# Performance work log

Measured on AMD Instinct MI355X. Metric: run time of the kernel, lower is better.

Reference implementation:

```python
import math
import jax, jax.numpy as jnp
import numpy as np

L, D, H, F, V, S = 4, 1024, 16, 4096, 50257, 2048
HS = D // H
EPS = 1e-5
STD = 0.02


def setup_inputs() -> dict:
    key = jax.random.key(0)
    keys = iter(jax.random.split(key, 24))

    def rn(shape):
        return (jax.random.normal(next(keys), shape, jnp.float32) * STD)

    inp = {
        "input_ids": jax.random.randint(next(keys), (1, S), 0, V, dtype=jnp.int64),
        "tok_emb": rn((V, D)),
        "pos_emb": rn((S, D)),
        # per-layer stacked params; linear weights stored [in, out]
        "Wq": rn((L, D, D)), "bq": jnp.zeros((L, D)),
        "Wk": rn((L, D, D)), "bk": jnp.zeros((L, D)),
        "Wv": rn((L, D, D)), "bv": jnp.zeros((L, D)),
        "Wo": rn((L, D, D)), "bo": jnp.zeros((L, D)),
        "W1": rn((L, D, F)), "b1": jnp.zeros((L, F)),
        "W2": rn((L, F, D)), "b2": jnp.zeros((L, D)),
        "ln1w": jnp.ones((L, D)), "ln1b": jnp.zeros((L, D)),
        "ln2w": jnp.ones((L, D)), "ln2b": jnp.zeros((L, D)),
        "lnfw": jnp.ones((D,)), "lnfb": jnp.zeros((D,)),
        "lm_head": rn((V, D)),  # torch Linear weight layout [out, in]
    }
    return inp


def _layernorm(x, w, b):
    m = jnp.mean(x, axis=-1, keepdims=True)
    v = jnp.mean(jnp.square(x - m), axis=-1, keepdims=True)
    return (x - m) * jax.lax.rsqrt(v + EPS) * w + b


def reference(input_ids, tok_emb, pos_emb, Wq, bq, Wk, bk, Wv, bv, Wo, bo,
              W1, b1, W2, b2, ln1w, ln1b, ln2w, ln2b, lnfw, lnfb, lm_head):
    B, Sq = input_ids.shape
    h = tok_emb[input_ids] + pos_emb[None, :Sq]  # [B,S,D]
    causal = jnp.tril(jnp.ones((Sq, Sq), dtype=bool))
    scale = 1.0 / math.sqrt(HS)

    def block(h, p):
        wq, bq_, wk, bk_, wv, bv_, wo, bo_, w1, b1_, w2, b2_, l1w, l1b, l2w, l2b = p
        x = _layernorm(h, l1w, l1b)
        q = (x @ wq + bq_).reshape(B, Sq, H, HS).transpose(0, 2, 1, 3)
        k = (x @ wk + bk_).reshape(B, Sq, H, HS).transpose(0, 2, 1, 3)
        v = (x @ wv + bv_).reshape(B, Sq, H, HS).transpose(0, 2, 1, 3)
        scores = jnp.einsum('bhqd,bhkd->bhqk', q, k) * scale
        scores = jnp.where(causal, scores, jnp.finfo(scores.dtype).min)
        attn = jax.nn.softmax(scores, axis=-1)  # dropout is identity at eval
        out = jnp.einsum('bhqk,bhkd->bhqd', attn, v)
        out = out.transpose(0, 2, 1, 3).reshape(B, Sq, D)
        h = h + out @ wo + bo_
        x = _layernorm(h, l2w, l2b)
        h = h + jax.nn.gelu(x @ w1 + b1_, approximate=False) @ w2 + b2_
        return h, None

    h, _ = jax.lax.scan(block, h, (Wq, bq, Wk, bk, Wv, bv, Wo, bo,
                                   W1, b1, W2, b2, ln1w, ln1b, ln2w, ln2b))
    h = _layernorm(h, lnfw, lnfb)
    logits = h @ lm_head.T  # [B,S,V]
    return logits
```

## Files before the change

### kernel.cpp

```cpp
#include <hip/hip_runtime.h>
#include <math.h>
#include <stdint.h>


#define SEQ 2048
#define DIM 1024
#define NHEAD 16
#define FFN 4096
#define VOCAB 50257
#define NLAYER 4
#define LNEPS 1e-5f
#define QKVD 3072
#define KVB 128

using bf16x8 = __attribute__((ext_vector_type(8))) short;
using s16x4  = __attribute__((ext_vector_type(4))) short;
using f32x4  = __attribute__((ext_vector_type(4))) float;
using fl4    = __attribute__((ext_vector_type(4))) float;

static __device__ __forceinline__ short f2bf(float f) {
  uint32_t u = __float_as_uint(f);
  u = (u + 0x7fffu + ((u >> 16) & 1u)) >> 16;
  return (short)u;
}
static __device__ __forceinline__ float bf2f(short s) {
  return __uint_as_float(((uint32_t)(uint16_t)s) << 16);
}
static __device__ __forceinline__ void gload_lds16(const void* g, void* l) {
  __builtin_amdgcn_global_load_lds((const __attribute__((address_space(1))) void*)g,
                                   (__attribute__((address_space(3))) void*)l, 16, 0, 0);
}

__global__ void embed_kernel(const int* __restrict__ ids,
                             const float* __restrict__ tok,
                             const float* __restrict__ pos,
                             float* __restrict__ h) {
  int i = blockIdx.x * blockDim.x + threadIdx.x;
  if (i < SEQ * DIM) {
    int s = i / DIM, d = i % DIM;
    h[i] = tok[(long)ids[s] * DIM + d] + pos[i];
  }
}

__global__ void ln_kernel(const float* __restrict__ x, const float* __restrict__ w,
                          const float* __restrict__ b, short* __restrict__ y) {
  int row = blockIdx.x;
  const float* xr = x + (long)row * DIM;
  short* yr = y + (long)row * DIM;
  int tid = threadIdx.x;
  float v0 = xr[tid], v1 = xr[tid + 256], v2 = xr[tid + 512], v3 = xr[tid + 768];
  __shared__ float red[8];
  float s = v0 + v1 + v2 + v3;
#pragma unroll
  for (int o = 32; o >= 1; o >>= 1) s += __shfl_xor(s, o);
  if ((tid & 63) == 0) red[tid >> 6] = s;
  __syncthreads();
  float mean = (red[0] + red[1] + red[2] + red[3]) * (1.f / DIM);
  float d0 = v0 - mean, d1 = v1 - mean, d2 = v2 - mean, d3 = v3 - mean;
  float q = d0 * d0 + d1 * d1 + d2 * d2 + d3 * d3;
#pragma unroll
  for (int o = 32; o >= 1; o >>= 1) q += __shfl_xor(q, o);
  if ((tid & 63) == 0) red[4 + (tid >> 6)] = q;
  __syncthreads();
  float var = (red[4] + red[5] + red[6] + red[7]) * (1.f / DIM);
  float rstd = rsqrtf(var + LNEPS);
  yr[tid]       = f2bf(d0 * rstd * w[tid] + b[tid]);
  yr[tid + 256] = f2bf(d1 * rstd * w[tid + 256] + b[tid + 256]);
  yr[tid + 512] = f2bf(d2 * rstd * w[tid + 512] + b[tid + 512]);
  yr[tid + 768] = f2bf(d3 * rstd * w[tid + 768] + b[tid + 768]);
}

__global__ void reduce_ln(const float* __restrict__ part, const float* __restrict__ bias,
                          const float* __restrict__ lnw, const float* __restrict__ lnb,
                          float* __restrict__ h, short* __restrict__ x) {
  const long MN = (long)SEQ * DIM;
  int row = blockIdx.x, tid = threadIdx.x;
  long off = (long)row * DIM + tid * 4;
  fl4 hv = *(const fl4*)(h + off);
  fl4 p0 = *(const fl4*)(part + off);
  fl4 p1 = *(const fl4*)(part + MN + off);
  fl4 bv = *(const fl4*)(bias + tid * 4);
  float v[4];
#pragma unroll
  for (int u = 0; u < 4; u++) v[u] = hv[u] + p0[u] + p1[u] + bv[u];
  __shared__ float red[8];
  float s = v[0] + v[1] + v[2] + v[3];
#pragma unroll
  for (int o = 32; o >= 1; o >>= 1) s += __shfl_xor(s, o);
  if ((tid & 63) == 0) red[tid >> 6] = s;
  __syncthreads();
  float mean = (red[0] + red[1] + red[2] + red[3]) * (1.f / DIM);
  float d[4], q = 0.f;
#pragma unroll
  for (int u = 0; u < 4; u++) { d[u] = v[u] - mean; q += d[u] * d[u]; }
#pragma unroll
  for (int o = 32; o >= 1; o >>= 1) q += __shfl_xor(q, o);
  if ((tid & 63) == 0) red[4 + (tid >> 6)] = q;
  fl4 hw; hw[0] = v[0]; hw[1] = v[1]; hw[2] = v[2]; hw[3] = v[3];
  *(fl4*)(h + off) = hw;
  __syncthreads();
  float var = (red[4] + red[5] + red[6] + red[7]) * (1.f / DIM);
  float rstd = rsqrtf(var + LNEPS);
  fl4 w = *(const fl4*)(lnw + tid * 4);
  fl4 bb = *(const fl4*)(lnb + tid * 4);
  s16x4 o;
#pragma unroll
  for (int u = 0; u < 4; u++) o[u] = f2bf(d[u] * rstd * w[u] + bb[u]);
  *(s16x4*)(x + off) = o;
}

__global__ void transpose64(const float* __restrict__ in, short* __restrict__ out,
                            int K, int N) {
  __shared__ float ts[64][65];
  int c0 = blockIdx.x * 64, r0 = blockIdx.y * 64;
  int tid = threadIdx.x;
  int lr = tid >> 4, lc4 = (tid & 15) * 4;
#pragma unroll
  for (int i = 0; i < 4; i++) {
    fl4 v = *(const fl4*)(in + (long)(r0 + lr + i * 16) * N + c0 + lc4);
    ts[lr + i * 16][lc4] = v[0]; ts[lr + i * 16][lc4 + 1] = v[1];
    ts[lr + i * 16][lc4 + 2] = v[2]; ts[lr + i * 16][lc4 + 3] = v[3];
  }
  __syncthreads();
#pragma unroll
  for (int i = 0; i < 2; i++) {
    int oc = (tid >> 3) + i * 32, seg = tid & 7;
    bf16x8 o;
#pragma unroll
    for (int u = 0; u < 8; u++) o[u] = f2bf(ts[seg * 8 + u][oc]);
    *(bf16x8*)(out + (long)(c0 + oc) * K + r0 + seg * 8) = o;
  }
}

struct TW4 { const float* src[4]; short* dst[4]; };
__global__ void transpose64_b4(TW4 p) {
  const float* in = p.src[blockIdx.z];
  short* out = p.dst[blockIdx.z];
  __shared__ float ts[64][65];
  int c0 = blockIdx.x * 64, r0 = blockIdx.y * 64;
  int tid = threadIdx.x;
  int lr = tid >> 4, lc4 = (tid & 15) * 4;
#pragma unroll
  for (int i = 0; i < 4; i++) {
    fl4 v = *(const fl4*)(in + (long)(r0 + lr + i * 16) * DIM + c0 + lc4);
    ts[lr + i * 16][lc4] = v[0]; ts[lr + i * 16][lc4 + 1] = v[1];
    ts[lr + i * 16][lc4 + 2] = v[2]; ts[lr + i * 16][lc4 + 3] = v[3];
  }
  __syncthreads();
#pragma unroll
  for (int i = 0; i < 2; i++) {
    int oc = (tid >> 3) + i * 32, seg = tid & 7;
    bf16x8 o;
#pragma unroll
    for (int u = 0; u < 8; u++) o[u] = f2bf(ts[seg * 8 + u][oc]);
    *(bf16x8*)(out + (long)(c0 + oc) * DIM + r0 + seg * 8) = o;
  }
}

__global__ void transpose_v(const short* __restrict__ qkv, short* __restrict__ vt) {
  __shared__ short t[64][72];
  int s0 = blockIdx.x * 64, c0 = blockIdx.y * 64;
  int tid = threadIdx.x;
#pragma unroll
  for (int i = 0; i < 2; i++) {
    int ca = i * 256 + tid;
    int row = ca >> 3, cp = ca & 7;
    bf16x8 v = *(const bf16x8*)(qkv + (long)(s0 + row) * QKVD + 2 * DIM + c0 + cp * 8);
    *(bf16x8*)&t[row][cp * 8] = v;
  }
  __syncthreads();
#pragma unroll
  for (int i = 0; i < 2; i++) {
    int ca = i * 256 + tid;
    int crow = ca >> 3, sp = ca & 7;
    bf16x8 o;
#pragma unroll
    for (int u = 0; u < 8; u++) o[u] = t[sp * 8 + u][crow];
    *(bf16x8*)(vt + (long)(c0 + crow) * SEQ + s0 + sp * 8) = o;
  }
}

__global__ void conv_bf16(const float* __restrict__ in, short* __restrict__ out, long n4) {
  long i = (long)blockIdx.x * blockDim.x + threadIdx.x;
  long stride = (long)gridDim.x * blockDim.x;
  for (; i < n4; i += stride) {
    fl4 v = *(const fl4*)(in + i * 4);
    s16x4 o;
    o[0] = f2bf(v[0]); o[1] = f2bf(v[1]); o[2] = f2bf(v[2]); o[3] = f2bf(v[3]);
    *(s16x4*)(out + i * 4) = o;
  }
}

__global__ void bias_cat(const float* __restrict__ bq, const float* __restrict__ bk,
                         const float* __restrict__ bv, float* __restrict__ out) {
  int i = blockIdx.x * 256 + threadIdx.x;
  if (i < QKVD) out[i] = i < DIM ? bq[i] : (i < 2 * DIM ? bk[i - DIM] : bv[i - 2 * DIM]);
}

template <bool GELU, bool BIAS, bool OUTBF16, int KS, bool XCDSWZ>
__global__ __launch_bounds__(256, 4) void gemm_small(
    const short* __restrict__ A, const short* __restrict__ Bt,
    const float* __restrict__ bias, void* __restrict__ Cout, int N, int Kfull) {
  __shared__ short lds[3][(64 + 128) * 32];
  const int tid = threadIdx.x, wid = tid >> 6, lane = tid & 63;
  const int l16 = lane & 15, lg = lane >> 4;
  int bx = blockIdx.x, by = blockIdx.y;
  if (XCDSWZ) {
    int gx = gridDim.x, nwg = gx * gridDim.y;
    int flat = by * gx + bx;
    int nf = (flat & 7) * (nwg >> 3) + (flat >> 3);
    bx = nf % gx; by = nf / gx;
  }
  const long m0 = (long)bx * 64, n0 = (long)by * 128;
  const int K = Kfull / KS;
  const int kbase = blockIdx.z * K;
  const int NT = K / 32;
  const int wm = wid >> 1, wn = wid & 1;

#define STG(t, b)                                                               \
  {                                                                             \
    short* As_ = lds[b];                                                        \
    short* Bs_ = lds[b] + 64 * 32;                                              \
    int kk_ = kbase + (t) * 32;                                                 \
    {                                                                           \
      int row_ = tid >> 2, cp_ = tid & 3, c_ = cp_ ^ ((row_ >> 1) & 3);         \
      gload_lds16(A + (m0 + row_) * (long)Kfull + kk_ + c_ * 8,                 \
                  As_ + (wid * 64) * 8);                                        \
    }                                                                           \
    _Pragma("unroll")                                                           \
    for (int i_ = 0; i_ < 2; i_++) {                                            \
      int ca_ = i_ * 256 + tid;                                                 \
      int row_ = ca_ >> 2, cp_ = ca_ & 3, c_ = cp_ ^ ((row_ >> 1) & 3);         \
      gload_lds16(Bt + (long)(n0 + row_) * Kfull + kk_ + c_ * 8,                \
                  Bs_ + (i_ * 256 + wid * 64) * 8);                             \
    }                                                                           \
  }

  f32x4 acc[2][4] = {};
  STG(0, 0);
  STG(1, 1);
  asm volatile("s_waitcnt vmcnt(3)" ::: "memory");
  __builtin_amdgcn_s_barrier();
  __builtin_amdgcn_sched_barrier(0);

  for (int t = 0; t < NT; t++) {
    const int b = t % 3;
    if (t + 2 < NT) STG(t + 2, (t + 2) % 3);
    const short* As = lds[b];
    const short* Bs = lds[b] + 64 * 32;
    bf16x8 af[2], bfr[4];
#pragma unroll
    for (int m = 0; m < 2; m++) {
      int row = wm * 32 + m * 16 + l16;
      af[m] = *(const bf16x8*)((const char*)As + row * 64 + ((lg ^ ((row >> 1) & 3)) * 16));
    }
#pragma unroll
    for (int n = 0; n < 4; n++) {
      int row = wn * 64 + n * 16 + l16;
      bfr[n] = *(const bf16x8*)((const char*)Bs + row * 64 + ((lg ^ ((row >> 1) & 3)) * 16));
    }
    __builtin_amdgcn_s_setprio(1);
#pragma unroll
    for (int m = 0; m < 2; m++)
#pragma unroll
      for (int n = 0; n < 4; n++)
        acc[m][n] = __builtin_amdgcn_mfma_f32_16x16x32_bf16(af[m], bfr[n], acc[m][n], 0, 0, 0);
    __builtin_amdgcn_s_setprio(0);
    if (t + 2 < NT) {
      asm volatile("s_waitcnt vmcnt(3)" ::: "memory");
    } else if (t + 1 < NT) {
      asm volatile("s_waitcnt vmcnt(0)" ::: "memory");
    }
    if (t + 1 < NT) {
      __builtin_amdgcn_s_barrier();
      __builtin_amdgcn_sched_barrier(0);
    }
  }
#undef STG

  const int lr4 = lg * 4;
  if (KS == 1) {
#pragma unroll
    for (int m = 0; m < 2; m++)
#pragma unroll
      for (int n = 0; n < 4; n++)
#pragma unroll
        for (int r = 0; r < 4; r++) {
          long row = m0 + wm * 32 + m * 16 + lr4 + r;
          long col = n0 + wn * 64 + n * 16 + l16;
          float v = acc[m][n][r];
          if (BIAS) v += bias[col];
          if (GELU) v = 0.5f * v * (1.f + erff(v * 0.70710678118f));
          if (OUTBF16) ((short*)Cout)[row * (long)N + col] = f2bf(v);
          else ((float*)Cout)[row * (long)N + col] = v;
        }
  } else {
    long M = (long)gridDim.x * 64;
    float* P = (float*)Cout + (long)blockIdx.z * M * N;
#pragma unroll
    for (int m = 0; m < 2; m++)
#pragma unroll
      for (int n = 0; n < 4; n++)
#pragma unroll
        for (int r = 0; r < 4; r++) {
          long row = m0 + wm * 32 + m * 16 + lr4 + r;
          long col = n0 + wn * 64 + n * 16 + l16;
          P[row * (long)N + col] = acc[m][n][r];
        }
  }
}

template <bool GELU, bool BIAS, bool OUTBF16, bool XCDSWZ>
__global__ __launch_bounds__(256, 3) void gemm4(
    const short* __restrict__ A, const short* __restrict__ Bt,
    const float* __restrict__ bias, void* __restrict__ Cout, int N, int Kfull) {
  __shared__ short lds[3][(128 + 128) * 32];
  const int tid = threadIdx.x, wid = tid >> 6, lane = tid & 63;
  const int l16 = lane & 15, lg = lane >> 4;
  int bx = blockIdx.x, by = blockIdx.y;
  if (XCDSWZ) {
    int gx = gridDim.x, nwg = gx * gridDim.y;
    int flat = by * gx + bx;
    int nf = (flat & 7) * (nwg >> 3) + (flat >> 3);
    bx = nf % gx; by = nf / gx;
  }
  const long m0 = (long)bx * 128, n0 = (long)by * 128;
  const int NT = Kfull / 32;
  const int wr = (wid >> 1) * 64, wc = (wid & 1) * 64;

#define STAGE4(t, b)                                                            \
  {                                                                             \
    short* As_ = lds[b];                                                        \
    short* Bs_ = lds[b] + 128 * 32;                                             \
    int kk_ = (t) * 32;                                                         \
    _Pragma("unroll")                                                           \
    for (int i_ = 0; i_ < 2; i_++) {                                            \
      int ca_ = i_ * 256 + tid;                                                 \
      int row_ = ca_ >> 2, cp_ = ca_ & 3, c_ = cp_ ^ ((row_ >> 1) & 3);         \
      gload_lds16(A + (m0 + row_) * (long)Kfull + kk_ + c_ * 8,                 \
                  As_ + (i_ * 256 + wid * 64) * 8);                             \
    }                                                                           \
    _Pragma("unroll")                                                           \
    for (int i_ = 0; i_ < 2; i_++) {                                            \
      int ca_ = i_ * 256 + tid;                                                 \
      int row_ = ca_ >> 2, cp_ = ca_ & 3, c_ = cp_ ^ ((row_ >> 1) & 3);         \
      gload_lds16(Bt + (long)(n0 + row_) * Kfull + kk_ + c_ * 8,                \
                  Bs_ + (i_ * 256 + wid * 64) * 8);                             \
    }                                                                           \
  }

  f32x4 acc[4][4] = {};
  STAGE4(0, 0);
  STAGE4(1, 1);
  asm volatile("s_waitcnt vmcnt(4)" ::: "memory");
  __builtin_amdgcn_s_barrier();
  __builtin_amdgcn_sched_barrier(0);

  for (int t = 0; t < NT; t++) {
    const int b = t % 3;
    if (t + 2 < NT) STAGE4(t + 2, (t + 2) % 3);
    const short* As = lds[b];
    const short* Bs = lds[b] + 128 * 32;
    bf16x8 af[4], bfr[4];
#pragma unroll
    for (int m = 0; m < 4; m++) {
      int row = wr + m * 16 + l16;
      af[m] = *(const bf16x8*)((const char*)As + row * 64 + ((lg ^ ((row >> 1) & 3)) * 16));
    }
#pragma unroll
    for (int n = 0; n < 4; n++) {
      int row = wc + n * 16 + l16;
      bfr[n] = *(const bf16x8*)((const char*)Bs + row * 64 + ((lg ^ ((row >> 1) & 3)) * 16));
    }
    __builtin_amdgcn_s_setprio(1);
#pragma unroll
    for (int m = 0; m < 4; m++)
#pragma unroll
      for (int n = 0; n < 4; n++)
        acc[m][n] = __builtin_amdgcn_mfma_f32_16x16x32_bf16(af[m], bfr[n], acc[m][n], 0, 0, 0);
    __builtin_amdgcn_s_setprio(0);
    if (t + 2 < NT) {
      asm volatile("s_waitcnt vmcnt(4)" ::: "memory");
    } else if (t + 1 < NT) {
      asm volatile("s_waitcnt vmcnt(0)" ::: "memory");
    }
    if (t + 1 < NT) {
      __builtin_amdgcn_s_barrier();
      __builtin_amdgcn_sched_barrier(0);
    }
  }
#undef STAGE4

  const int lr4 = lg * 4;
#pragma unroll
  for (int m = 0; m < 4; m++)
#pragma unroll
    for (int n = 0; n < 4; n++)
#pragma unroll
      for (int r = 0; r < 4; r++) {
        long row = m0 + wr + m * 16 + lr4 + r;
        long col = n0 + wc + n * 16 + l16;
        float v = acc[m][n][r];
        if (BIAS) v += bias[col];
        if (GELU) v = 0.5f * v * (1.f + erff(v * 0.70710678118f));
        if (OUTBF16) ((short*)Cout)[row * (long)N + col] = f2bf(v);
        else ((float*)Cout)[row * (long)N + col] = v;
      }
}

template <bool XCDSWZ>
__global__ __launch_bounds__(512, 2) void gemm256(
    const short* __restrict__ A, const short* __restrict__ Bt,
    float* __restrict__ C, int N, int K) {
  __shared__ short ldsA[2][256 * 64];
  __shared__ short ldsB[2][256 * 64];
  const int tid = threadIdx.x, wid = tid >> 6, lane = tid & 63;
  const int l16 = lane & 15, lg = lane >> 4;
  const int wm = wid >> 2, wn = wid & 3;
  int bx = blockIdx.x, by = blockIdx.y;
  if (XCDSWZ) {
    int gx = gridDim.x, nwg = gx * gridDim.y;
    int flat = by * gx + bx;
    int nf = (flat & 7) * (nwg >> 3) + (flat >> 3);
    bx = nf % gx; by = nf / gx;
  }
  const long m0 = (long)bx * 256, n0 = (long)by * 256;
  const int NT = K / 64;

  auto SA = [&](int t, int b, int r0) {
    int row = r0 + wid * 8 + (lane >> 3);
    int c = (lane & 7) ^ (row & 7);
    gload_lds16(A + (m0 + row) * (long)K + t * 64 + c * 8,
                &ldsA[b][(r0 + wid * 8) * 64]);
  };
  auto SB = [&](int t, int b, int r0) {
    int row = r0 + wid * 8 + (lane >> 3);
    int c = (lane & 7) ^ (row & 7);
    int rowb = (int)n0 + row;
    if (rowb > N - 1) rowb = N - 1;
    gload_lds16(Bt + (long)rowb * K + t * 64 + c * 8,
                &ldsB[b][(r0 + wid * 8) * 64]);
  };

  f32x4 acc[8][4] = {};
  bf16x8 bfr[4][2];

  auto PH = [&](int b, int q) {
    bf16x8 af[2][2];
    if (q == 0) {
#pragma unroll
      for (int nf = 0; nf < 4; nf++) {
        int row = wn * 64 + nf * 16 + l16;
#pragma unroll
        for (int ks = 0; ks < 2; ks++)
          bfr[nf][ks] = *(const bf16x8*)((const char*)&ldsB[b][0] + row * 128 +
                                         (((ks * 4 + lg) ^ (row & 7)) * 16));
      }
    }
#pragma unroll
    for (int j = 0; j < 2; j++) {
      int row = wm * 128 + (q * 2 + j) * 16 + l16;
#pragma unroll
      for (int ks = 0; ks < 2; ks++)
        af[j][ks] = *(const bf16x8*)((const char*)&ldsA[b][0] + row * 128 +
                                     (((ks * 4 + lg) ^ (row & 7)) * 16));
    }
    __builtin_amdgcn_s_barrier();
    __builtin_amdgcn_s_setprio(1);
#pragma unroll
    for (int ks = 0; ks < 2; ks++)
#pragma unroll
      for (int j = 0; j < 2; j++)
#pragma unroll
        for (int nf = 0; nf < 4; nf++)
          acc[q * 2 + j][nf] =
              __builtin_amdgcn_mfma_f32_16x16x32_bf16(af[j][ks], bfr[nf][ks],
                                                      acc[q * 2 + j][nf], 0, 0, 0);
    __builtin_amdgcn_s_setprio(0);
  };

  SA(0, 0, 0); SA(0, 0, 64); SA(0, 0, 128); SA(0, 0, 192);
  SB(0, 0, 0); SB(0, 0, 64); SB(0, 0, 128); SB(0, 0, 192);
  SA(1, 1, 0); SA(1, 1, 128);
  asm volatile("s_waitcnt vmcnt(2)" ::: "memory");
  __builtin_amdgcn_s_barrier();

  for (int i = 0; i < NT / 2; i++) {
    const int e = 2 * i, o = e + 1;
    const bool more = (e + 2) < NT;
    SA(o, 1, 64); SA(o, 1, 192);
    PH(0, 0);
    __builtin_amdgcn_s_barrier();
    SB(o, 1, 0); SB(o, 1, 64);
    PH(0, 1);
    __builtin_amdgcn_s_barrier();
    SB(o, 1, 128); SB(o, 1, 192);
    PH(0, 2);
    __builtin_amdgcn_s_barrier();
    if (more) { SA(e + 2, 0, 0); SA(e + 2, 0, 128); }
    PH(0, 3);
    if (more) asm volatile("s_waitcnt vmcnt(2)" ::: "memory");
    else      asm volatile("s_waitcnt vmcnt(0)" ::: "memory");
    __builtin_amdgcn_s_barrier();
    if (more) { SA(e + 2, 0, 64); SA(e + 2, 0, 192); }
    PH(1, 0);
    __builtin_amdgcn_s_barrier();
    if (more) { SB(e + 2, 0, 0); SB(e + 2, 0, 64); }
    PH(1, 1);
    __builtin_amdgcn_s_barrier();
    if (more) { SB(e + 2, 0, 128); SB(e + 2, 0, 192); }
    PH(1, 2);
    __builtin_amdgcn_s_barrier();
    if (more) { SA(e + 3, 1, 0); SA(e + 3, 1, 128); }
    PH(1, 3);
    if (more) {
      asm volatile("s_waitcnt vmcnt(2)" ::: "memory");
      __builtin_amdgcn_s_barrier();
    }
  }

#pragma unroll
  for (int mf = 0; mf < 8; mf++)
#pragma unroll
    for (int nf = 0; nf < 4; nf++)
#pragma unroll
      for (int r = 0; r < 4; r++) {
        long row = m0 + wm * 128 + mf * 16 + lg * 4 + r;
        long col = n0 + wn * 64 + nf * 16 + l16;
        if (col < N) C[row * (long)N + col] = acc[mf][nf][r];
      }
}

__global__ __launch_bounds__(256) void attn_mfma(const short* __restrict__ qkv,
                                                 const short* __restrict__ vtg,
                                                 short* __restrict__ Oa) {
  int hh = blockIdx.x, qb = blockIdx.y;
  int q0 = qb * 64;
  int tid = threadIdx.x, wv = tid >> 6, lane = tid & 63;
  int l16 = lane & 15, lg = lane >> 4;
  int hcol = hh * 64;
  __shared__ short Ks[2][KVB * 64];
  __shared__ short Vt[2][64 * KVB];
  __shared__ short Pl[4][16 * KVB];

  bf16x8 qf[2];
  {
    const short* qrow = qkv + (long)(q0 + wv * 16 + l16) * QKVD + hcol;
#pragma unroll
    for (int dc = 0; dc < 2; dc++) {
      bf16x8 t = *(const bf16x8*)(qrow + dc * 32 + lg * 8);
#pragma unroll
      for (int j = 0; j < 8; j++) t[j] = f2bf(bf2f(t[j]) * 0.125f);
      qf[dc] = t;
    }
  }
  f32x4 of[4] = {};
  float mrun[4], lrun[4];
#pragma unroll
  for (int r = 0; r < 4; r++) { mrun[r] = -3e38f; lrun[r] = 0.f; }

#define STAGEKV(kt_, b_)                                                        \
  {                                                                             \
    int k0_ = (kt_) * KVB;                                                      \
    _Pragma("unroll")                                                           \
    for (int i = 0; i < 4; i++) {                                               \
      int ca = i * 256 + tid;                                                   \
      int row = ca >> 3, cp = ca & 7, c = cp ^ (row & 7);                       \
      gload_lds16(qkv + (long)(k0_ + row) * QKVD + DIM + hcol + c * 8,          \
                  (short*)Ks[b_] + (i * 256 + wv * 64) * 8);                    \
    }                                                                           \
    _Pragma("unroll")                                                           \
    for (int i = 0; i < 4; i++) {                                               \
      int ca = i * 256 + tid;                                                   \
      int row = ca >> 4, cp = ca & 15, c = cp ^ (row & 7);                      \
      gload_lds16(vtg + (long)(hcol + row) * SEQ + k0_ + c * 8,                 \
                  (short*)Vt[b_] + (i * 256 + wv * 64) * 8);                    \
    }                                                                           \
  }

  int nt = qb / 2 + 1;
  STAGEKV(0, 0);
  asm volatile("s_waitcnt vmcnt(0)" ::: "memory");
  __builtin_amdgcn_s_barrier();

  for (int kt = 0; kt < nt; kt++) {
    const int cur = kt & 1;
    if (kt + 1 < nt) STAGEKV(kt + 1, cur ^ 1);
    int k0 = kt * KVB;

    f32x4 sacc[8] = {};
#pragma unroll
    for (int kc = 0; kc < 8; kc++) {
      int row = kc * 16 + l16;
#pragma unroll
      for (int dc = 0; dc < 2; dc++) {
        bf16x8 kf = *(const bf16x8*)((const char*)Ks[cur] + row * 128 + (((dc * 4 + lg) ^ (row & 7)) * 16));
        sacc[kc] = __builtin_amdgcn_mfma_f32_16x16x32_bf16(qf[dc], kf, sacc[kc], 0, 0, 0);
      }
    }

    float sv[8][4], pf[8][4];
#pragma unroll
    for (int kc = 0; kc < 8; kc++)
#pragma unroll
      for (int r = 0; r < 4; r++) sv[kc][r] = sacc[kc][r];
    if (kt == nt - 1) {
#pragma unroll
      for (int kc = 0; kc < 8; kc++)
#pragma unroll
        for (int r = 0; r < 4; r++) {
          int kg = k0 + kc * 16 + l16;
          int rg = q0 + wv * 16 + lg * 4 + r;
          if (kg > rg) sv[kc][r] = -3e38f;
        }
    }
    float corr[4];
#pragma unroll
    for (int r = 0; r < 4; r++) {
      float m01 = fmaxf(sv[0][r], sv[1][r]), m23 = fmaxf(sv[2][r], sv[3][r]);
      float m45 = fmaxf(sv[4][r], sv[5][r]), m67 = fmaxf(sv[6][r], sv[7][r]);
      float mt = fmaxf(fmaxf(m01, m23), fmaxf(m45, m67));
#pragma unroll
      for (int o = 8; o >= 1; o >>= 1) mt = fmaxf(mt, __shfl_xor(mt, o));
      float mn = fmaxf(mrun[r], mt);
      corr[r] = __expf(mrun[r] - mn);
      mrun[r] = mn;
      float ps = 0.f;
#pragma unroll
      for (int kc = 0; kc < 8; kc++) {
        float p = __expf(sv[kc][r] - mn);
        pf[kc][r] = p;
        ps += p;
      }
#pragma unroll
      for (int o = 8; o >= 1; o >>= 1) ps += __shfl_xor(ps, o);
      lrun[r] = lrun[r] * corr[r] + ps;
    }
#pragma unroll
    for (int c = 0; c < 4; c++)
#pragma unroll
      for (int r = 0; r < 4; r++) of[c][r] *= corr[r];
#pragma unroll
    for (int kc = 0; kc < 8; kc++)
#pragma unroll
      for (int r = 0; r < 4; r++) {
        int row = lg * 4 + r, col = kc * 16 + l16;
        int chunk = col >> 3;
        *(short*)((char*)Pl[wv] + row * 256 + ((chunk ^ (row & 7)) * 16) + (col & 7) * 2) = f2bf(pf[kc][r]);
      }
    bf16x8 pfr[4];
#pragma unroll
    for (int kc2 = 0; kc2 < 4; kc2++) {
      int cl = kc2 * 4 + lg;
      pfr[kc2] = *(const bf16x8*)((const char*)Pl[wv] + l16 * 256 + ((cl ^ (l16 & 7)) * 16));
    }
#pragma unroll
    for (int c = 0; c < 4; c++)
#pragma unroll
      for (int kc2 = 0; kc2 < 4; kc2++) {
        int vrow = c * 16 + l16;
        int cl = kc2 * 4 + lg;
        bf16x8 vf = *(const bf16x8*)((const char*)Vt[cur] + vrow * 256 + ((cl ^ (vrow & 7)) * 16));
        of[c] = __builtin_amdgcn_mfma_f32_16x16x32_bf16(pfr[kc2], vf, of[c], 0, 0, 0);
      }
    if (kt + 1 < nt) {
      asm volatile("s_waitcnt vmcnt(0)" ::: "memory");
      __builtin_amdgcn_s_barrier();
      __builtin_amdgcn_sched_barrier(0);
    }
  }
#undef STAGEKV
#pragma unroll
  for (int c = 0; c < 4; c++)
#pragma unroll
    for (int r = 0; r < 4; r++) {
      int rowg = q0 + wv * 16 + lg * 4 + r;
      int colg = hcol + c * 16 + l16;
      Oa[(long)rowg * DIM + colg] = f2bf(of[c][r] / lrun[r]);
    }
}

extern "C" void kernel_launch(void* const* d_in, const int* in_sizes, int n_in,
                              void* d_out, int out_size, void* d_ws, size_t ws_size,
                              hipStream_t stream) {
  const int* ids = (const int*)d_in[0];
  const float* tok = (const float*)d_in[1];
  const float* pos = (const float*)d_in[2];
  const float* Wq = (const float*)d_in[3];
  const float* bq = (const float*)d_in[4];
  const float* Wk = (const float*)d_in[5];
  const float* bk = (const float*)d_in[6];
  const float* Wv = (const float*)d_in[7];
  const float* bv = (const float*)d_in[8];
  const float* Wo = (const float*)d_in[9];
  const float* bo = (const float*)d_in[10];
  const float* W1 = (const float*)d_in[11];
  const float* b1 = (const float*)d_in[12];
  const float* W2 = (const float*)d_in[13];
  const float* b2 = (const float*)d_in[14];
  const float* ln1w = (const float*)d_in[15];
  const float* ln1b = (const float*)d_in[16];
  const float* ln2w = (const float*)d_in[17];
  const float* ln2b = (const float*)d_in[18];
  const float* lnfw = (const float*)d_in[19];
  const float* lnfb = (const float*)d_in[20];
  const float* lmh = (const float*)d_in[21];
  float* out = (float*)d_out;

  char* wsb = (char*)d_ws;
  float* h = (float*)wsb;
  short* x = (short*)(wsb + 8388608);
  char* big = wsb + 8388608 + 4194304;
  short* qkv  = (short*)big;
  short* a    = (short*)(big + 12582912);
  short* vt   = (short*)(big + 16777216);
  short* fbuf = (short*)(big + 20971520);
  float* pproj = (float*)fbuf;
  float* pffn2 = (float*)big;
  char* wdyn = big + 37748736;
  short* wqkvT = (short*)wdyn;
  short* woT   = (short*)(wdyn + 6291456);
  short* w1T   = (short*)(wdyn + 8388608);
  short* w2T   = (short*)(wdyn + 16777216);
  float* bias3 = (float*)(wdyn + 25165824);
  short* lmhB = (short*)big;

  embed_kernel<<<(SEQ * DIM + 255) / 256, 256, 0, stream>>>(ids, tok, pos, h);
  ln_kernel<<<SEQ, 256, 0, stream>>>(h, ln1w, ln1b, x);

  dim3 gQKV(SEQ / 64, QKVD / 128);
  dim3 gPROJ(SEQ / 64, DIM / 128, 2);
  dim3 gFFN1(SEQ / 128, FFN / 128);
  dim3 gFFN2(SEQ / 64, DIM / 128, 2);
  dim3 gV(SEQ / 256, (VOCAB + 255) / 256);

  for (int l = 0; l < NLAYER; l++) {
    TW4 tw;
    tw.src[0] = Wq + (long)l * DIM * DIM; tw.dst[0] = wqkvT;
    tw.src[1] = Wk + (long)l * DIM * DIM; tw.dst[1] = wqkvT + (long)DIM * DIM;
    tw.src[2] = Wv + (long)l * DIM * DIM; tw.dst[2] = wqkvT + (long)2 * DIM * DIM;
    tw.src[3] = Wo + (long)l * DIM * DIM; tw.dst[3] = woT;
    transpose64_b4<<<dim3(16, 16, 4), 256, 0, stream>>>(tw);
    transpose64<<<dim3(64, 16), 256, 0, stream>>>(W1 + (long)l * DIM * FFN, w1T, DIM, FFN);
    transpose64<<<dim3(16, 64), 256, 0, stream>>>(W2 + (long)l * FFN * DIM, w2T, FFN, DIM);
    bias_cat<<<12, 256, 0, stream>>>(bq + (long)l * DIM, bk + (long)l * DIM, bv + (long)l * DIM, bias3);

    gemm_small<false, true, true, 1, true><<<gQKV, 256, 0, stream>>>(x, wqkvT, bias3, qkv, QKVD, DIM);
    transpose_v<<<dim3(SEQ / 64, DIM / 64), 256, 0, stream>>>(qkv, vt);
    attn_mfma<<<dim3(NHEAD, SEQ / 64), 256, 0, stream>>>(qkv, vt, a);
    gemm_small<false, false, false, 2, true><<<gPROJ, 256, 0, stream>>>(a, woT, nullptr, pproj, DIM, DIM);
    reduce_ln<<<SEQ, 256, 0, stream>>>(pproj, bo + (long)l * DIM,
                                       ln2w + (long)l * DIM, ln2b + (long)l * DIM, h, x);
    gemm4<true, true, true, true><<<gFFN1, 256, 0, stream>>>(x, w1T, b1 + (long)l * FFN, fbuf, FFN, DIM);
    gemm_small<false, false, false, 2, true><<<gFFN2, 256, 0, stream>>>(fbuf, w2T, nullptr, pffn2, DIM, FFN);
    const float* nw = (l < NLAYER - 1) ? ln1w + (long)(l + 1) * DIM : lnfw;
    const float* nb = (l < NLAYER - 1) ? ln1b + (long)(l + 1) * DIM : lnfb;
    reduce_ln<<<SEQ, 256, 0, stream>>>(pffn2, b2 + (long)l * DIM, nw, nb, h, x);
  }

  conv_bf16<<<2048, 256, 0, stream>>>(lmh, lmhB, (long)VOCAB * DIM / 4);
  gemm256<true><<<gV, 512, 0, stream>>>(x, lmhB, out, VOCAB, DIM);
}
```

Measured before the change: 1.138 ms.

## Make LM-head GEMM persistent, fuse weight prep kernels, raise MFMA priority in attention

The LM-head GEMM becomes a persistent kernel with 256 blocks. Each block walks its output tiles in a single continuous pipeline, prefetching the next tile's K-slices while it finishes the current one, which hides tile-boundary bubbles and the tail effect. The per-layer weight transposes and the bias concatenation merge into one prep launch to cut launch overhead. Attention raises wave priority around its MFMA sections. The persistent kernel runs at occupancy 1 and its tile order mapping is untested at the vocab boundary, so performance could move either way.

```diff
diff --git a/kernel.cpp b/kernel.cpp
--- a/kernel.cpp
+++ b/kernel.cpp
@@ -109,15 +109,38 @@
   *(s16x4*)(x + off) = o;
 }
 
-__global__ void transpose64(const float* __restrict__ in, short* __restrict__ out,
-                            int K, int N) {
+struct Prep {
+  const float *wq, *wk, *wv, *wo, *w1, *w2, *bq, *bk, *bv;
+  short *qkvT, *woT, *w1T, *w2T;
+  float* bias3;
+};
+__global__ void prep_kernel(Prep p) {
+  int t = blockIdx.x;
+  if (t >= 3072) {
+    for (int k = threadIdx.x; k < QKVD; k += 256)
+      p.bias3[k] = k < DIM ? p.bq[k] : (k < 2 * DIM ? p.bk[k - DIM] : p.bv[k - 2 * DIM]);
+    return;
+  }
+  const float* in; short* out; int Kd, Nd, r0, c0;
+  if (t < 1024) {
+    int m = t >> 8, lt = t & 255;
+    const float* srcs[4] = {p.wq, p.wk, p.wv, p.wo};
+    short* dsts[4] = {p.qkvT, p.qkvT + (long)DIM * DIM, p.qkvT + (long)2 * DIM * DIM, p.woT};
+    in = srcs[m]; out = dsts[m]; Kd = DIM; Nd = DIM;
+    c0 = (lt & 15) * 64; r0 = (lt >> 4) * 64;
+  } else if (t < 2048) {
+    int lt = t - 1024; in = p.w1; out = p.w1T; Kd = DIM; Nd = FFN;
+    c0 = (lt & 63) * 64; r0 = (lt >> 6) * 64;
+  } else {
+    int lt = t - 2048; in = p.w2; out = p.w2T; Kd = FFN; Nd = DIM;
+    c0 = (lt & 15) * 64; r0 = (lt >> 4) * 64;
+  }
   __shared__ float ts[64][65];
-  int c0 = blockIdx.x * 64, r0 = blockIdx.y * 64;
   int tid = threadIdx.x;
   int lr = tid >> 4, lc4 = (tid & 15) * 4;
 #pragma unroll
   for (int i = 0; i < 4; i++) {
-    fl4 v = *(const fl4*)(in + (long)(r0 + lr + i * 16) * N + c0 + lc4);
+    fl4 v = *(const fl4*)(in + (long)(r0 + lr + i * 16) * Nd + c0 + lc4);
     ts[lr + i * 16][lc4] = v[0]; ts[lr + i * 16][lc4 + 1] = v[1];
     ts[lr + i * 16][lc4 + 2] = v[2]; ts[lr + i * 16][lc4 + 3] = v[3];
   }
@@ -128,32 +151,7 @@
     bf16x8 o;
 #pragma unroll
     for (int u = 0; u < 8; u++) o[u] = f2bf(ts[seg * 8 + u][oc]);
-    *(bf16x8*)(out + (long)(c0 + oc) * K + r0 + seg * 8) = o;
-  }
-}
-
-struct TW4 { const float* src[4]; short* dst[4]; };
-__global__ void transpose64_b4(TW4 p) {
-  const float* in = p.src[blockIdx.z];
-  short* out = p.dst[blockIdx.z];
-  __shared__ float ts[64][65];
-  int c0 = blockIdx.x * 64, r0 = blockIdx.y * 64;
-  int tid = threadIdx.x;
-  int lr = tid >> 4, lc4 = (tid & 15) * 4;
-#pragma unroll
-  for (int i = 0; i < 4; i++) {
-    fl4 v = *(const fl4*)(in + (long)(r0 + lr + i * 16) * DIM + c0 + lc4);
-    ts[lr + i * 16][lc4] = v[0]; ts[lr + i * 16][lc4 + 1] = v[1];
-    ts[lr + i * 16][lc4 + 2] = v[2]; ts[lr + i * 16][lc4 + 3] = v[3];
-  }
-  __syncthreads();
-#pragma unroll
-  for (int i = 0; i < 2; i++) {
-    int oc = (tid >> 3) + i * 32, seg = tid & 7;
-    bf16x8 o;
-#pragma unroll
-    for (int u = 0; u < 8; u++) o[u] = f2bf(ts[seg * 8 + u][oc]);
-    *(bf16x8*)(out + (long)(c0 + oc) * DIM + r0 + seg * 8) = o;
+    *(bf16x8*)(out + (long)(c0 + oc) * Kd + r0 + seg * 8) = o;
   }
 }
 
@@ -189,12 +187,6 @@
     o[0] = f2bf(v[0]); o[1] = f2bf(v[1]); o[2] = f2bf(v[2]); o[3] = f2bf(v[3]);
     *(s16x4*)(out + i * 4) = o;
   }
-}
-
-__global__ void bias_cat(const float* __restrict__ bq, const float* __restrict__ bk,
-                         const float* __restrict__ bv, float* __restrict__ out) {
-  int i = blockIdx.x * 256 + threadIdx.x;
-  if (i < QKVD) out[i] = i < DIM ? bq[i] : (i < 2 * DIM ? bk[i - DIM] : bv[i - 2 * DIM]);
 }
 
 template <bool GELU, bool BIAS, bool OUTBF16, int KS, bool XCDSWZ>
@@ -408,38 +400,38 @@
       }
 }
 
-template <bool XCDSWZ>
-__global__ __launch_bounds__(512, 2) void gemm256(
+__global__ __launch_bounds__(512, 1) void gemm256p(
     const short* __restrict__ A, const short* __restrict__ Bt,
-    float* __restrict__ C, int N, int K) {
+    float* __restrict__ C, int N, int K, int totTiles) {
   __shared__ short ldsA[2][256 * 64];
   __shared__ short ldsB[2][256 * 64];
   const int tid = threadIdx.x, wid = tid >> 6, lane = tid & 63;
   const int l16 = lane & 15, lg = lane >> 4;
   const int wm = wid >> 2, wn = wid & 3;
-  int bx = blockIdx.x, by = blockIdx.y;
-  if (XCDSWZ) {
-    int gx = gridDim.x, nwg = gx * gridDim.y;
-    int flat = by * gx + bx;
-    int nf = (flat & 7) * (nwg >> 3) + (flat >> 3);
-    bx = nf % gx; by = nf / gx;
-  }
-  const long m0 = (long)bx * 256, n0 = (long)by * 256;
-  const int NT = K / 64;
-
-  auto SA = [&](int t, int b, int r0) {
+  const int bid = blockIdx.x, nb = gridDim.x;
+  const int ntiles = (totTiles - bid + nb - 1) / nb;
+  const int TOT = ntiles * 16;
+
+  auto tileMN = [&](int ord, long& m0, long& n0) {
+    int j = bid + ord * nb;
+    m0 = (long)(j & 7) * 256;
+    n0 = (long)(j >> 3) * 256;
+  };
+  auto SA = [&](int s, int r0) {
+    long m0s, n0s; tileMN(s >> 4, m0s, n0s);
     int row = r0 + wid * 8 + (lane >> 3);
     int c = (lane & 7) ^ (row & 7);
-    gload_lds16(A + (m0 + row) * (long)K + t * 64 + c * 8,
-                &ldsA[b][(r0 + wid * 8) * 64]);
+    gload_lds16(A + (m0s + row) * (long)K + (s & 15) * 64 + c * 8,
+                &ldsA[s & 1][(r0 + wid * 8) * 64]);
   };
-  auto SB = [&](int t, int b, int r0) {
+  auto SB = [&](int s, int r0) {
+    long m0s, n0s; tileMN(s >> 4, m0s, n0s);
     int row = r0 + wid * 8 + (lane >> 3);
     int c = (lane & 7) ^ (row & 7);
-    int rowb = (int)n0 + row;
+    int rowb = (int)n0s + row;
     if (rowb > N - 1) rowb = N - 1;
-    gload_lds16(Bt + (long)rowb * K + t * 64 + c * 8,
-                &ldsB[b][(r0 + wid * 8) * 64]);
+    gload_lds16(Bt + (long)rowb * K + (s & 15) * 64 + c * 8,
+                &ldsB[s & 1][(r0 + wid * 8) * 64]);
   };
 
   f32x4 acc[8][4] = {};
@@ -479,56 +471,61 @@
     __builtin_amdgcn_s_setprio(0);
   };
 
-  SA(0, 0, 0); SA(0, 0, 64); SA(0, 0, 128); SA(0, 0, 192);
-  SB(0, 0, 0); SB(0, 0, 64); SB(0, 0, 128); SB(0, 0, 192);
-  SA(1, 1, 0); SA(1, 1, 128);
+  SA(0, 0); SA(0, 64); SA(0, 128); SA(0, 192);
+  SB(0, 0); SB(0, 64); SB(0, 128); SB(0, 192);
+  SA(1, 0); SA(1, 128);
   asm volatile("s_waitcnt vmcnt(2)" ::: "memory");
   __builtin_amdgcn_s_barrier();
 
-  for (int i = 0; i < NT / 2; i++) {
-    const int e = 2 * i, o = e + 1;
-    const bool more = (e + 2) < NT;
-    SA(o, 1, 64); SA(o, 1, 192);
+  for (int it = 0; it < TOT / 2; it++) {
+    const int e = 2 * it, o = e + 1;
+    const bool more = (e + 2) < TOT;
+    SA(o, 64); SA(o, 192);
     PH(0, 0);
     __builtin_amdgcn_s_barrier();
-    SB(o, 1, 0); SB(o, 1, 64);
+    SB(o, 0); SB(o, 64);
     PH(0, 1);
     __builtin_amdgcn_s_barrier();
-    SB(o, 1, 128); SB(o, 1, 192);
+    SB(o, 128); SB(o, 192);
     PH(0, 2);
     __builtin_amdgcn_s_barrier();
-    if (more) { SA(e + 2, 0, 0); SA(e + 2, 0, 128); }
+    if (more) { SA(e + 2, 0); SA(e + 2, 128); }
     PH(0, 3);
     if (more) asm volatile("s_waitcnt vmcnt(2)" ::: "memory");
     else      asm volatile("s_waitcnt vmcnt(0)" ::: "memory");
     __builtin_amdgcn_s_barrier();
-    if (more) { SA(e + 2, 0, 64); SA(e + 2, 0, 192); }
+    if (more) { SA(e + 2, 64); SA(e + 2, 192); }
     PH(1, 0);
     __builtin_amdgcn_s_barrier();
-    if (more) { SB(e + 2, 0, 0); SB(e + 2, 0, 64); }
+    if (more) { SB(e + 2, 0); SB(e + 2, 64); }
     PH(1, 1);
     __builtin_amdgcn_s_barrier();
-    if (more) { SB(e + 2, 0, 128); SB(e + 2, 0, 192); }
+    if (more) { SB(e + 2, 128); SB(e + 2, 192); }
     PH(1, 2);
     __builtin_amdgcn_s_barrier();
-    if (more) { SA(e + 3, 1, 0); SA(e + 3, 1, 128); }
+    if (more) { SA(e + 3, 0); SA(e + 3, 128); }
     PH(1, 3);
     if (more) {
       asm volatile("s_waitcnt vmcnt(2)" ::: "memory");
       __builtin_amdgcn_s_barrier();
-    }
-  }
-
-#pragma unroll
-  for (int mf = 0; mf < 8; mf++)
-#pragma unroll
-    for (int nf = 0; nf < 4; nf++)
-#pragma unroll
-      for (int r = 0; r < 4; r++) {
-        long row = m0 + wm * 128 + mf * 16 + lg * 4 + r;
-        long col = n0 + wn * 64 + nf * 16 + l16;
-        if (col < N) C[row * (long)N + col] = acc[mf][nf][r];
-      }
+    } else {
+      asm volatile("s_waitcnt vmcnt(0)" ::: "memory");
+    }
+    if ((o & 15) == 15) {
+      long m0c, n0c; tileMN(o >> 4, m0c, n0c);
+#pragma unroll
+      for (int mf = 0; mf < 8; mf++)
+#pragma unroll
+        for (int nf = 0; nf < 4; nf++)
+#pragma unroll
+          for (int r = 0; r < 4; r++) {
+            long row = m0c + wm * 128 + mf * 16 + lg * 4 + r;
+            long col = n0c + wn * 64 + nf * 16 + l16;
+            if (col < N) C[row * (long)N + col] = acc[mf][nf][r];
+            acc[mf][nf][r] = 0.f;
+          }
+    }
+  }
 }
 
 __global__ __launch_bounds__(256) void attn_mfma(const short* __restrict__ qkv,
@@ -589,6 +586,7 @@
     int k0 = kt * KVB;
 
     f32x4 sacc[8] = {};
+    __builtin_amdgcn_s_setprio(1);
 #pragma unroll
     for (int kc = 0; kc < 8; kc++) {
       int row = kc * 16 + l16;
@@ -598,6 +596,7 @@
         sacc[kc] = __builtin_amdgcn_mfma_f32_16x16x32_bf16(qf[dc], kf, sacc[kc], 0, 0, 0);
       }
     }
+    __builtin_amdgcn_s_setprio(0);
 
     float sv[8][4], pf[8][4];
 #pragma unroll
@@ -654,6 +653,7 @@
       int cl = kc2 * 4 + lg;
       pfr[kc2] = *(const bf16x8*)((const char*)Pl[wv] + l16 * 256 + ((cl ^ (l16 & 7)) * 16));
     }
+    __builtin_amdgcn_s_setprio(1);
 #pragma unroll
     for (int c = 0; c < 4; c++)
 #pragma unroll
@@ -663,6 +663,7 @@
         bf16x8 vf = *(const bf16x8*)((const char*)Vt[cur] + vrow * 256 + ((cl ^ (vrow & 7)) * 16));
         of[c] = __builtin_amdgcn_mfma_f32_16x16x32_bf16(pfr[kc2], vf, of[c], 0, 0, 0);
       }
+    __builtin_amdgcn_s_setprio(0);
     if (kt + 1 < nt) {
       asm volatile("s_waitcnt vmcnt(0)" ::: "memory");
       __builtin_amdgcn_s_barrier();
@@ -732,18 +733,15 @@
   dim3 gPROJ(SEQ / 64, DIM / 128, 2);
   dim3 gFFN1(SEQ / 128, FFN / 128);
   dim3 gFFN2(SEQ / 64, DIM / 128, 2);
-  dim3 gV(SEQ / 256, (VOCAB + 255) / 256);
 
   for (int l = 0; l < NLAYER; l++) {
-    TW4 tw;
-    tw.src[0] = Wq + (long)l * DIM * DIM; tw.dst[0] = wqkvT;
-    tw.src[1] = Wk + (long)l * DIM * DIM; tw.dst[1] = wqkvT + (long)DIM * DIM;
-    tw.src[2] = Wv + (long)l * DIM * DIM; tw.dst[2] = wqkvT + (long)2 * DIM * DIM;
-    tw.src[3] = Wo + (long)l * DIM * DIM; tw.dst[3] = woT;
-    transpose64_b4<<<dim3(16, 16, 4), 256, 0, stream>>>(tw);
-    transpose64<<<dim3(64, 16), 256, 0, stream>>>(W1 + (long)l * DIM * FFN, w1T, DIM, FFN);
-    transpose64<<<dim3(16, 64), 256, 0, stream>>>(W2 + (long)l * FFN * DIM, w2T, FFN, DIM);
-    bias_cat<<<12, 256, 0, stream>>>(bq + (long)l * DIM, bk + (long)l * DIM, bv + (long)l * DIM, bias3);
+    Prep p;
+    p.wq = Wq + (long)l * DIM * DIM; p.wk = Wk + (long)l * DIM * DIM;
+    p.wv = Wv + (long)l * DIM * DIM; p.wo = Wo + (long)l * DIM * DIM;
+    p.w1 = W1 + (long)l * DIM * FFN; p.w2 = W2 + (long)l * FFN * DIM;
+    p.bq = bq + (long)l * DIM; p.bk = bk + (long)l * DIM; p.bv = bv + (long)l * DIM;
+    p.qkvT = wqkvT; p.woT = woT; p.w1T = w1T; p.w2T = w2T; p.bias3 = bias3;
+    prep_kernel<<<3073, 256, 0, stream>>>(p);
 
     gemm_small<false, true, true, 1, true><<<gQKV, 256, 0, stream>>>(x, wqkvT, bias3, qkv, QKVD, DIM);
     transpose_v<<<dim3(SEQ / 64, DIM / 64), 256, 0, stream>>>(qkv, vt);
@@ -759,5 +757,6 @@
   }
 
   conv_bf16<<<2048, 256, 0, stream>>>(lmh, lmhB, (long)VOCAB * DIM / 4);
-  gemm256<true><<<gV, 512, 0, stream>>>(x, lmhB, out, VOCAB, DIM);
-}
+  gemm256p<<<dim3(256), 512, 0, stream>>>(x, lmhB, out, VOCAB, DIM,
+                                          (SEQ / 256) * ((VOCAB + 255) / 256));
+}
```

After: 1.118 ms. About the same (-1.8%).
